# Kernel tuning notes

Measured on AMD Instinct MI355X. Metric: run time of the kernel, lower is better.

The kernel has to match this reference:

```python
import jax, jax.numpy as jnp
import numpy as np

N = 50000          # nodes
E = 1600000        # edges (avg degree 32)
NUM_FEAT = 512
HIDDEN = 128
NUM_CLASS = 40
NUM_LAYERS = 4
EPS = 0.3


def setup_inputs() -> dict:
    key = jax.random.key(0)
    ks = jax.random.split(key, 8)
    x = jax.random.normal(ks[0], (N, NUM_FEAT), dtype=jnp.float32)
    edge_index = jax.random.randint(ks[1], (2, E), 0, N, dtype=jnp.int64)
    gain = 1.414  # xavier_normal_(gain=1.414) as in reset_parameters
    W1 = jax.random.normal(ks[2], (HIDDEN, NUM_FEAT), dtype=jnp.float32) * gain * (2.0 / (HIDDEN + NUM_FEAT)) ** 0.5
    b1 = jnp.zeros((HIDDEN,), dtype=jnp.float32)
    W2 = jax.random.normal(ks[3], (NUM_CLASS, HIDDEN), dtype=jnp.float32) * gain * (2.0 / (NUM_CLASS + HIDDEN)) ** 0.5
    b2 = jnp.zeros((NUM_CLASS,), dtype=jnp.float32)
    # FAConv attention vectors: Linear(channels, 1, bias=False) per layer
    att_l = jax.random.normal(ks[4], (NUM_LAYERS, HIDDEN), dtype=jnp.float32) * (2.0 / (1 + HIDDEN)) ** 0.5
    att_r = jax.random.normal(ks[5], (NUM_LAYERS, HIDDEN), dtype=jnp.float32) * (2.0 / (1 + HIDDEN)) ** 0.5
    return dict(x=x, edge_index=edge_index, W1=W1, b1=b1, W2=W2, b2=b2, att_l=att_l, att_r=att_r)


def reference(x, edge_index, W1, b1, W2, b2, att_l, att_r):
    n = x.shape[0]
    # gcn_norm with self-loops (FAConv default add_self_loops=True)
    loops = jnp.arange(n, dtype=edge_index.dtype)
    src = jnp.concatenate([edge_index[0], loops])  # source j
    dst = jnp.concatenate([edge_index[1], loops])  # target i
    deg = jax.ops.segment_sum(jnp.ones_like(src, dtype=x.dtype), dst, num_segments=n)
    dis = jax.lax.rsqrt(jnp.maximum(deg, 1.0))
    norm = dis[src] * dis[dst]  # [E+N]

    # eval mode: dropout is identity
    h = jax.nn.relu(x @ W1.T + b1)  # [N, HIDDEN]
    raw = h
    for l in range(NUM_LAYERS):
        al = h @ att_l[l]  # [N]
        ar = h @ att_r[l]  # [N]
        coef = jnp.tanh(al[src] + ar[dst]) * norm            # [E+N]
        agg = jax.ops.segment_sum(h[src] * coef[:, None], dst, num_segments=n)
        h = agg + EPS * raw
    logits = h @ W2.T + b2  # [N, NUM_CLASS]
    return jax.nn.log_softmax(logits, axis=1)
```

## Files before the change

kernel.cpp:

```cpp
#include <hip/hip_runtime.h>
#include <cmath>


#define HIDDEN 128
#define FEAT 512
#define NCLASS 40
#define LDST 40
#define NB 256
#define PITCH 12544

typedef __attribute__((ext_vector_type(8))) short short8;
typedef __attribute__((ext_vector_type(4))) float f32x4;

__device__ __forceinline__ float bf_lo(unsigned u) { return __uint_as_float(u << 16); }
__device__ __forceinline__ float bf_hi(unsigned u) { return __uint_as_float(u & 0xffff0000u); }
__device__ __forceinline__ unsigned pack_bf16(float x, float y) {
    unsigned ux = __float_as_uint(x);
    unsigned uy = __float_as_uint(y);
    unsigned lx = (ux + 0x7fffu + ((ux >> 16) & 1u)) >> 16;
    unsigned hy = (uy + 0x7fffu + ((uy >> 16) & 1u)) & 0xffff0000u;
    return hy | lx;
}
__device__ __forceinline__ float fast_tanh(float x) {
    x = fminf(fmaxf(x, -15.f), 15.f);
    float e = __expf(2.f * x);
    return (e - 1.f) / (e + 1.f);
}

__global__ __launch_bounds__(256) void k_hist(const int* __restrict__ ei, int E, int CE,
                                              unsigned* __restrict__ partial,
                                              ushort* __restrict__ lrank) {
    __shared__ unsigned lh[PITCH];
    const int b = blockIdx.x, tid = threadIdx.x;
    for (int w = tid; w < PITCH; w += 256) lh[w] = 0;
    __syncthreads();
    int e0 = b * CE, e1 = min(E, e0 + CE);
    for (int e = e0 + tid; e < e1; e += 256) {
        int dst = ei[E + e];
        int sh = (dst & 3) * 8;
        unsigned old = atomicAdd(&lh[dst >> 2], 1u << sh);
        lrank[e] = (ushort)((old >> sh) & 0xffu);
    }
    __syncthreads();
    unsigned* prow = partial + (size_t)b * PITCH;
    for (int w = tid; w < PITCH; w += 256) prow[w] = lh[w];
}

__global__ void k_hscan(unsigned* __restrict__ partial, int* __restrict__ deg, int n) {
    int w = blockIdx.x * 256 + threadIdx.x;
    if (w >= PITCH) return;
    unsigned run = 0;
    size_t idx = w;
    for (int b = 0; b < NB; ++b, idx += PITCH) {
        unsigned v = partial[idx];
        partial[idx] = run;
        run += v;
    }
    int node = 4 * w;
    if (node < n)     deg[node]     = run & 0xffu;
    if (node + 1 < n) deg[node + 1] = (run >> 8) & 0xffu;
    if (node + 2 < n) deg[node + 2] = (run >> 16) & 0xffu;
    if (node + 3 < n) deg[node + 3] = run >> 24;
}

__global__ void k_dis(const int* __restrict__ deg, float* __restrict__ dis, int n) {
    int i = blockIdx.x * 256 + threadIdx.x;
    if (i < n) dis[i] = rsqrtf((float)(deg[i] + 1));
}

__global__ void k_scan1(const int* __restrict__ deg, int* __restrict__ offs,
                        int* __restrict__ part, int n) {
    __shared__ int s[256];
    int tid = threadIdx.x;
    int gid = blockIdx.x * 256 + tid;
    int v = (gid < n) ? deg[gid] : 0;
    s[tid] = v;
    __syncthreads();
    for (int off = 1; off < 256; off <<= 1) {
        int t = (tid >= off) ? s[tid - off] : 0;
        __syncthreads();
        s[tid] += t;
        __syncthreads();
    }
    if (gid < n) offs[gid] = s[tid] - v;
    if (tid == 255) part[blockIdx.x] = s[255];
}

__global__ void k_scan2(int* __restrict__ part, int nb) {
    __shared__ int s[256];
    int tid = threadIdx.x;
    int v = (tid < nb) ? part[tid] : 0;
    s[tid] = v;
    __syncthreads();
    for (int off = 1; off < 256; off <<= 1) {
        int t = (tid >= off) ? s[tid - off] : 0;
        __syncthreads();
        s[tid] += t;
        __syncthreads();
    }
    if (tid < nb) part[tid] = s[tid] - v;
}

__global__ void k_scan3(int* __restrict__ offs, const int* __restrict__ part, int n, int E) {
    int gid = blockIdx.x * 256 + threadIdx.x;
    if (gid < n) offs[gid] += part[blockIdx.x];
    if (gid == 0) offs[n] = E;
}

__global__ __launch_bounds__(256) void k_csr_fill(const int* __restrict__ ei, int E, int CE,
                                                  const int* __restrict__ offs,
                                                  const unsigned* __restrict__ partial,
                                                  const ushort* __restrict__ lrank,
                                                  int* __restrict__ csrc) {
    __shared__ unsigned lp[PITCH];
    const int b = blockIdx.x, tid = threadIdx.x;
    const unsigned* prow = partial + (size_t)b * PITCH;
    for (int w = tid; w < PITCH; w += 256) lp[w] = prow[w];
    __syncthreads();
    int e0 = b * CE, e1 = min(E, e0 + CE);
    for (int e = e0 + tid; e < e1; e += 256) {
        int dst = ei[E + e];
        int src = ei[e];
        unsigned wv = lp[dst >> 2];
        int base = (wv >> ((dst & 3) * 8)) & 0xffu;
        csrc[offs[dst] + base + (int)lrank[e]] = src;
    }
}

__global__ __launch_bounds__(256) void k_gemm1(const float* __restrict__ x,
                                               const float* __restrict__ W1,
                                               const float* __restrict__ b1,
                                               float* __restrict__ h, int M) {
    __shared__ ushort As[128 * LDST];
    __shared__ ushort Bs[128 * LDST];
    const int tid = threadIdx.x;
    const int bm = blockIdx.x * 128;
    const int wave = tid >> 6, lane = tid & 63;
    const int rh = (wave >> 1) * 64;
    const int ch = (wave & 1) * 64;
    const int sub = lane & 15, quad = lane >> 4;
    const int lrow = tid >> 3;
    const int lcol = (tid & 7) * 4;
    f32x4 acc[4][4] = {};
    for (int k0 = 0; k0 < FEAT; k0 += 32) {
#pragma unroll
        for (int i = 0; i < 4; ++i) {
            int r = lrow + 32 * i;
            int grow = bm + r;
            float4 v = make_float4(0.f, 0.f, 0.f, 0.f);
            if (grow < M) v = *(const float4*)(x + (size_t)grow * FEAT + k0 + lcol);
            uint2 pk = make_uint2(pack_bf16(v.x, v.y), pack_bf16(v.z, v.w));
            *(uint2*)(As + r * LDST + lcol) = pk;
        }
#pragma unroll
        for (int i = 0; i < 4; ++i) {
            int r = lrow + 32 * i;
            float4 v = *(const float4*)(W1 + (size_t)r * FEAT + k0 + lcol);
            uint2 pk = make_uint2(pack_bf16(v.x, v.y), pack_bf16(v.z, v.w));
            *(uint2*)(Bs + r * LDST + lcol) = pk;
        }
        __syncthreads();
        short8 af[4], bfr[4];
#pragma unroll
        for (int t = 0; t < 4; ++t)
            af[t] = *(const short8*)(As + (rh + t * 16 + sub) * LDST + quad * 8);
#pragma unroll
        for (int u = 0; u < 4; ++u)
            bfr[u] = *(const short8*)(Bs + (ch + u * 16 + sub) * LDST + quad * 8);
#pragma unroll
        for (int t = 0; t < 4; ++t)
#pragma unroll
            for (int u = 0; u < 4; ++u)
                acc[t][u] = __builtin_amdgcn_mfma_f32_16x16x32_bf16(af[t], bfr[u], acc[t][u], 0, 0, 0);
        __syncthreads();
    }
    float b1v[4];
#pragma unroll
    for (int u = 0; u < 4; ++u) b1v[u] = b1[ch + u * 16 + sub];
#pragma unroll
    for (int t = 0; t < 4; ++t) {
#pragma unroll
        for (int u = 0; u < 4; ++u) {
            int col = ch + u * 16 + sub;
#pragma unroll
            for (int r2 = 0; r2 < 4; ++r2) {
                int grow = bm + rh + t * 16 + quad * 4 + r2;
                if (grow < M)
                    h[(size_t)grow * HIDDEN + col] = fmaxf(acc[t][u][r2] + b1v[u], 0.f);
            }
        }
    }
}

__global__ void k_prep(const float* __restrict__ h, unsigned* __restrict__ hbf,
                       const float* __restrict__ attl, const float* __restrict__ attr,
                       const float* __restrict__ dis, float2* __restrict__ al2,
                       float* __restrict__ ar, int n) {
    int node = (blockIdx.x * blockDim.x + threadIdx.x) >> 6;
    int lane = threadIdx.x & 63;
    if (node >= n) return;
    float2 hv = ((const float2*)(h + (size_t)node * HIDDEN))[lane];
    hbf[(size_t)node * 64 + lane] = pack_bf16(hv.x, hv.y);
    float pl = hv.x * attl[2 * lane] + hv.y * attl[2 * lane + 1];
    float pr = hv.x * attr[2 * lane] + hv.y * attr[2 * lane + 1];
    for (int off = 32; off; off >>= 1) {
        pl += __shfl_down(pl, off);
        pr += __shfl_down(pr, off);
    }
    if (lane == 0) {
        al2[node] = make_float2(pl, dis[node]);
        ar[node] = pr;
    }
}

__global__ void k_aggregate(const unsigned* __restrict__ hbf, const float* __restrict__ raw,
                            const float2* __restrict__ al2, const float* __restrict__ ar,
                            const int* __restrict__ offs, const int* __restrict__ csrc,
                            float* __restrict__ hout, unsigned* __restrict__ houtbf,
                            const float* __restrict__ attl_n, const float* __restrict__ attr_n,
                            float2* __restrict__ al2_o, float* __restrict__ ar_o, int n) {
    int node = (blockIdx.x * blockDim.x + threadIdx.x) >> 6;
    int lane = threadIdx.x & 63;
    if (node >= n) return;
    const int grp = lane >> 4;
    const int sub = lane & 15;
    const float arn = ar[node];
    const float2 selfld = al2[node];
    const float disn = selfld.y;
    float acc[8] = {0.f, 0.f, 0.f, 0.f, 0.f, 0.f, 0.f, 0.f};
    int e0 = offs[node], e1 = offs[node + 1];
    int e = e0;
    for (; e + 16 <= e1; e += 16) {
        int smy = csrc[e + sub];
        float2 lmy = al2[smy];
        float cmy = fast_tanh(lmy.x + arn) * lmy.y * disn;
        int sa = __shfl(smy, grp);
        int sb = __shfl(smy, 4 + grp);
        int sc = __shfl(smy, 8 + grp);
        int sd = __shfl(smy, 12 + grp);
        float ca = __shfl(cmy, grp);
        float cb = __shfl(cmy, 4 + grp);
        float cc = __shfl(cmy, 8 + grp);
        float cd = __shfl(cmy, 12 + grp);
        uint4 ra = *(const uint4*)(hbf + (size_t)sa * 64 + sub * 4);
        uint4 rb = *(const uint4*)(hbf + (size_t)sb * 64 + sub * 4);
        uint4 rc = *(const uint4*)(hbf + (size_t)sc * 64 + sub * 4);
        uint4 rd = *(const uint4*)(hbf + (size_t)sd * 64 + sub * 4);
        acc[0] += ca * bf_lo(ra.x); acc[1] += ca * bf_hi(ra.x);
        acc[2] += ca * bf_lo(ra.y); acc[3] += ca * bf_hi(ra.y);
        acc[4] += ca * bf_lo(ra.z); acc[5] += ca * bf_hi(ra.z);
        acc[6] += ca * bf_lo(ra.w); acc[7] += ca * bf_hi(ra.w);
        acc[0] += cb * bf_lo(rb.x); acc[1] += cb * bf_hi(rb.x);
        acc[2] += cb * bf_lo(rb.y); acc[3] += cb * bf_hi(rb.y);
        acc[4] += cb * bf_lo(rb.z); acc[5] += cb * bf_hi(rb.z);
        acc[6] += cb * bf_lo(rb.w); acc[7] += cb * bf_hi(rb.w);
        acc[0] += cc * bf_lo(rc.x); acc[1] += cc * bf_hi(rc.x);
        acc[2] += cc * bf_lo(rc.y); acc[3] += cc * bf_hi(rc.y);
        acc[4] += cc * bf_lo(rc.z); acc[5] += cc * bf_hi(rc.z);
        acc[6] += cc * bf_lo(rc.w); acc[7] += cc * bf_hi(rc.w);
        acc[0] += cd * bf_lo(rd.x); acc[1] += cd * bf_hi(rd.x);
        acc[2] += cd * bf_lo(rd.y); acc[3] += cd * bf_hi(rd.y);
        acc[4] += cd * bf_lo(rd.z); acc[5] += cd * bf_hi(rd.z);
        acc[6] += cd * bf_lo(rd.w); acc[7] += cd * bf_hi(rd.w);
    }
    for (; e + 4 <= e1; e += 4) {
        int sa = csrc[e + grp];
        float2 la = al2[sa];
        uint4 ra = *(const uint4*)(hbf + (size_t)sa * 64 + sub * 4);
        float ca = fast_tanh(la.x + arn) * la.y * disn;
        acc[0] += ca * bf_lo(ra.x); acc[1] += ca * bf_hi(ra.x);
        acc[2] += ca * bf_lo(ra.y); acc[3] += ca * bf_hi(ra.y);
        acc[4] += ca * bf_lo(ra.z); acc[5] += ca * bf_hi(ra.z);
        acc[6] += ca * bf_lo(ra.w); acc[7] += ca * bf_hi(ra.w);
    }
#pragma unroll
    for (int j = 0; j < 8; ++j) {
        acc[j] += __shfl_xor(acc[j], 16);
        acc[j] += __shfl_xor(acc[j], 32);
    }
    for (; e < e1; ++e) {
        int s = csrc[e];
        float2 ls = al2[s];
        uint4 r = *(const uint4*)(hbf + (size_t)s * 64 + sub * 4);
        float c = fast_tanh(ls.x + arn) * ls.y * disn;
        acc[0] += c * bf_lo(r.x); acc[1] += c * bf_hi(r.x);
        acc[2] += c * bf_lo(r.y); acc[3] += c * bf_hi(r.y);
        acc[4] += c * bf_lo(r.z); acc[5] += c * bf_hi(r.z);
        acc[6] += c * bf_lo(r.w); acc[7] += c * bf_hi(r.w);
    }
    {
        float c = fast_tanh(selfld.x + arn) * disn * disn;
        uint4 r = *(const uint4*)(hbf + (size_t)node * 64 + sub * 4);
        acc[0] += c * bf_lo(r.x); acc[1] += c * bf_hi(r.x);
        acc[2] += c * bf_lo(r.y); acc[3] += c * bf_hi(r.y);
        acc[4] += c * bf_lo(r.z); acc[5] += c * bf_hi(r.z);
        acc[6] += c * bf_lo(r.w); acc[7] += c * bf_hi(r.w);
    }
    float o[8];
    {
        float4 rv0 = *(const float4*)(raw + (size_t)node * HIDDEN + sub * 8);
        float4 rv1 = *(const float4*)(raw + (size_t)node * HIDDEN + sub * 8 + 4);
        o[0] = acc[0] + 0.3f * rv0.x; o[1] = acc[1] + 0.3f * rv0.y;
        o[2] = acc[2] + 0.3f * rv0.z; o[3] = acc[3] + 0.3f * rv0.w;
        o[4] = acc[4] + 0.3f * rv1.x; o[5] = acc[5] + 0.3f * rv1.y;
        o[6] = acc[6] + 0.3f * rv1.z; o[7] = acc[7] + 0.3f * rv1.w;
    }
    if (grp == 0) {
        *(float4*)(hout + (size_t)node * HIDDEN + sub * 8) = make_float4(o[0], o[1], o[2], o[3]);
        *(float4*)(hout + (size_t)node * HIDDEN + sub * 8 + 4) = make_float4(o[4], o[5], o[6], o[7]);
        if (houtbf) {
            uint4 pk = make_uint4(pack_bf16(o[0], o[1]), pack_bf16(o[2], o[3]),
                                  pack_bf16(o[4], o[5]), pack_bf16(o[6], o[7]));
            *(uint4*)(houtbf + (size_t)node * 64 + sub * 4) = pk;
        }
    }
    if (attl_n) {
        float4 a0 = *(const float4*)(attl_n + sub * 8);
        float4 a1 = *(const float4*)(attl_n + sub * 8 + 4);
        float4 c0 = *(const float4*)(attr_n + sub * 8);
        float4 c1 = *(const float4*)(attr_n + sub * 8 + 4);
        float pl = o[0] * a0.x + o[1] * a0.y + o[2] * a0.z + o[3] * a0.w +
                   o[4] * a1.x + o[5] * a1.y + o[6] * a1.z + o[7] * a1.w;
        float pr = o[0] * c0.x + o[1] * c0.y + o[2] * c0.z + o[3] * c0.w +
                   o[4] * c1.x + o[5] * c1.y + o[6] * c1.z + o[7] * c1.w;
        for (int off = 8; off; off >>= 1) {
            pl += __shfl_xor(pl, off);
            pr += __shfl_xor(pr, off);
        }
        if (lane == 0) {
            al2_o[node] = make_float2(pl, disn);
            ar_o[node] = pr;
        }
    }
}

__global__ __launch_bounds__(256) void k_out(const float* __restrict__ h,
                                             const float* __restrict__ W2,
                                             const float* __restrict__ b2,
                                             float* __restrict__ out, int n) {
    __shared__ float ws[NCLASS * HIDDEN];
    __shared__ float bs[NCLASS];
    const int tid = threadIdx.x;
    for (int i = tid; i < NCLASS * HIDDEN / 4; i += 256)
        ((float4*)ws)[i] = ((const float4*)W2)[i];
    if (tid < NCLASS) bs[tid] = b2[tid];
    __syncthreads();
    int node = blockIdx.x * 128 + (tid >> 1);
    const int half = tid & 1;
    const int c0 = half * 20;
    if (node >= n) return;
    const float* hr = h + (size_t)node * HIDDEN;
    float acc[20];
#pragma unroll
    for (int c = 0; c < 20; ++c) acc[c] = bs[c0 + c];
#pragma unroll
    for (int k0 = 0; k0 < HIDDEN; k0 += 16) {
        float4 h0 = *(const float4*)(hr + k0);
        float4 h1 = *(const float4*)(hr + k0 + 4);
        float4 h2v = *(const float4*)(hr + k0 + 8);
        float4 h3 = *(const float4*)(hr + k0 + 12);
#pragma unroll
        for (int c = 0; c < 20; ++c) {
            const float* w = ws + (c0 + c) * HIDDEN + k0;
            float4 w0 = *(const float4*)(w);
            float4 w1 = *(const float4*)(w + 4);
            float4 w2v = *(const float4*)(w + 8);
            float4 w3 = *(const float4*)(w + 12);
            acc[c] += h0.x * w0.x + h0.y * w0.y + h0.z * w0.z + h0.w * w0.w +
                      h1.x * w1.x + h1.y * w1.y + h1.z * w1.z + h1.w * w1.w +
                      h2v.x * w2v.x + h2v.y * w2v.y + h2v.z * w2v.z + h2v.w * w2v.w +
                      h3.x * w3.x + h3.y * w3.y + h3.z * w3.z + h3.w * w3.w;
        }
    }
    float m = -INFINITY;
#pragma unroll
    for (int c = 0; c < 20; ++c) m = fmaxf(m, acc[c]);
    m = fmaxf(m, __shfl_xor(m, 1));
    float ssum = 0.f;
#pragma unroll
    for (int c = 0; c < 20; ++c) ssum += expf(acc[c] - m);
    ssum += __shfl_xor(ssum, 1);
    float lse = m + logf(ssum);
    float* orow = out + (size_t)node * NCLASS + c0;
#pragma unroll
    for (int c = 0; c < 20; ++c) orow[c] = acc[c] - lse;
}

extern "C" void kernel_launch(void* const* d_in, const int* in_sizes, int n_in,
                              void* d_out, int out_size, void* d_ws, size_t ws_size,
                              hipStream_t stream) {
    const float* x    = (const float*)d_in[0];
    const int*   ei   = (const int*)d_in[1];
    const float* W1   = (const float*)d_in[2];
    const float* b1   = (const float*)d_in[3];
    const float* W2   = (const float*)d_in[4];
    const float* b2   = (const float*)d_in[5];
    const float* attl = (const float*)d_in[6];
    const float* attr = (const float*)d_in[7];
    const int N = in_sizes[0] / FEAT;
    const int E = in_sizes[1] / 2;
    float* out = (float*)d_out;

    char* p = (char*)d_ws;
    auto take = [&](size_t bytes) {
        void* q = (void*)p;
        p += (bytes + 255) & ~(size_t)255;
        return q;
    };
    float*    h0   = (float*)take((size_t)N * HIDDEN * 4);
    float*    h1   = (float*)take((size_t)N * HIDDEN * 4);
    float*    h2   = (float*)take((size_t)N * HIDDEN * 4);
    unsigned* hb0  = (unsigned*)take((size_t)N * 64 * 4);
    unsigned* hb1  = (unsigned*)take((size_t)N * 64 * 4);
    int*      deg  = (int*)take((size_t)N * 4);
    float*    dis  = (float*)take((size_t)N * 4);
    int*      offs = (int*)take((size_t)(N + 1) * 4);
    unsigned* partial = (unsigned*)take((size_t)NB * PITCH * 4);
    ushort*   lrank   = (ushort*)take((size_t)E * 2);
    int*      csrc = (int*)take((size_t)E * 4);
    float2*   al2A = (float2*)take((size_t)N * 8);
    float2*   al2B = (float2*)take((size_t)N * 8);
    float*    arA  = (float*)take((size_t)N * 4);
    float*    arB  = (float*)take((size_t)N * 4);
    int*      part = (int*)take(1024);

    const int nbl = (N + 255) / 256;
    const int CE = (E + NB - 1) / NB;

    k_hist<<<NB, 256, 0, stream>>>(ei, E, CE, partial, lrank);
    k_hscan<<<(PITCH + 255) / 256, 256, 0, stream>>>(partial, deg, N);
    k_dis<<<nbl, 256, 0, stream>>>(deg, dis, N);
    k_scan1<<<nbl, 256, 0, stream>>>(deg, offs, part, N);
    k_scan2<<<1, 256, 0, stream>>>(part, nbl);
    k_scan3<<<nbl, 256, 0, stream>>>(offs, part, N, E);
    k_csr_fill<<<NB, 256, 0, stream>>>(ei, E, CE, offs, partial, lrank, csrc);

    k_gemm1<<<(N + 127) / 128, 256, 0, stream>>>(x, W1, b1, h0, N);
    k_prep<<<(N + 3) / 4, 256, 0, stream>>>(h0, hb0, attl, attr, dis, al2A, arA, N);

    float*    fout[4] = {h1, h2, h1, h2};
    unsigned* hbin = hb0, *hbout = hb1;
    float2*   alin = al2A, *alout = al2B;
    float*    arin = arA,  *arout = arB;
    for (int l = 0; l < 4; ++l) {
        const float* attl_n = (l < 3) ? (attl + (l + 1) * HIDDEN) : nullptr;
        const float* attr_n = (l < 3) ? (attr + (l + 1) * HIDDEN) : nullptr;
        unsigned* hbo = (l < 3) ? hbout : nullptr;
        k_aggregate<<<(N + 3) / 4, 256, 0, stream>>>(hbin, h0, alin, arin, offs, csrc,
                                                     fout[l], hbo, attl_n, attr_n,
                                                     alout, arout, N);
        unsigned* tb = hbin; hbin = hbout; hbout = tb;
        float2* ta = alin; alin = alout; alout = ta;
        float* tr = arin; arin = arout; arout = tr;
    }

    k_out<<<(N + 127) / 128, 256, 0, stream>>>(h2, W2, b2, out, N);
}
```

Before: 579.1 us.

## Halve GEMM1 row tile and prefetch next K-slice into registers

The first-layer GEMM kernel now uses 64-row tiles instead of 128, doubling the block count (about 782 blocks for 50000 nodes) to fill more compute units. It also software-pipelines the K loop by loading the next 32-wide slice of x and W1 into registers while the current slice's MFMAs run. The aim is to hide global-memory latency in a GEMM bound by bandwidth on reading x. In exchange, W1 is re-read by twice as many blocks and each block does less MFMA work per load.

```diff
diff --git a/kernel.cpp b/kernel.cpp
--- a/kernel.cpp
+++ b/kernel.cpp
@@ -8,6 +8,7 @@
 #define LDST 40
 #define NB 256
 #define PITCH 12544
+#define BM1 64
 
 typedef __attribute__((ext_vector_type(8))) short short8;
 typedef __attribute__((ext_vector_type(4))) float f32x4;
@@ -131,44 +132,59 @@
                                                const float* __restrict__ W1,
                                                const float* __restrict__ b1,
                                                float* __restrict__ h, int M) {
-    __shared__ ushort As[128 * LDST];
+    __shared__ ushort As[BM1 * LDST];
     __shared__ ushort Bs[128 * LDST];
     const int tid = threadIdx.x;
-    const int bm = blockIdx.x * 128;
+    const int bm = blockIdx.x * BM1;
     const int wave = tid >> 6, lane = tid & 63;
-    const int rh = (wave >> 1) * 64;
+    const int rh = (wave >> 1) * 32;
     const int ch = (wave & 1) * 64;
     const int sub = lane & 15, quad = lane >> 4;
     const int lrow = tid >> 3;
     const int lcol = (tid & 7) * 4;
-    f32x4 acc[4][4] = {};
+    f32x4 acc[2][4] = {};
+    float4 av[2], bv[4];
+#pragma unroll
+    for (int i = 0; i < 2; ++i) {
+        int grow = bm + lrow + 32 * i;
+        av[i] = (grow < M) ? *(const float4*)(x + (size_t)grow * FEAT + lcol)
+                           : make_float4(0.f, 0.f, 0.f, 0.f);
+    }
+#pragma unroll
+    for (int i = 0; i < 4; ++i)
+        bv[i] = *(const float4*)(W1 + (size_t)(lrow + 32 * i) * FEAT + lcol);
+
     for (int k0 = 0; k0 < FEAT; k0 += 32) {
 #pragma unroll
-        for (int i = 0; i < 4; ++i) {
-            int r = lrow + 32 * i;
-            int grow = bm + r;
-            float4 v = make_float4(0.f, 0.f, 0.f, 0.f);
-            if (grow < M) v = *(const float4*)(x + (size_t)grow * FEAT + k0 + lcol);
-            uint2 pk = make_uint2(pack_bf16(v.x, v.y), pack_bf16(v.z, v.w));
-            *(uint2*)(As + r * LDST + lcol) = pk;
-        }
-#pragma unroll
-        for (int i = 0; i < 4; ++i) {
-            int r = lrow + 32 * i;
-            float4 v = *(const float4*)(W1 + (size_t)r * FEAT + k0 + lcol);
-            uint2 pk = make_uint2(pack_bf16(v.x, v.y), pack_bf16(v.z, v.w));
-            *(uint2*)(Bs + r * LDST + lcol) = pk;
-        }
-        __syncthreads();
-        short8 af[4], bfr[4];
-#pragma unroll
-        for (int t = 0; t < 4; ++t)
+        for (int i = 0; i < 2; ++i)
+            *(uint2*)(As + (lrow + 32 * i) * LDST + lcol) =
+                make_uint2(pack_bf16(av[i].x, av[i].y), pack_bf16(av[i].z, av[i].w));
+#pragma unroll
+        for (int i = 0; i < 4; ++i)
+            *(uint2*)(Bs + (lrow + 32 * i) * LDST + lcol) =
+                make_uint2(pack_bf16(bv[i].x, bv[i].y), pack_bf16(bv[i].z, bv[i].w));
+        __syncthreads();
+        if (k0 + 32 < FEAT) {
+            const int kn = k0 + 32;
+#pragma unroll
+            for (int i = 0; i < 2; ++i) {
+                int grow = bm + lrow + 32 * i;
+                av[i] = (grow < M) ? *(const float4*)(x + (size_t)grow * FEAT + kn + lcol)
+                                   : make_float4(0.f, 0.f, 0.f, 0.f);
+            }
+#pragma unroll
+            for (int i = 0; i < 4; ++i)
+                bv[i] = *(const float4*)(W1 + (size_t)(lrow + 32 * i) * FEAT + kn + lcol);
+        }
+        short8 af[2], bfr[4];
+#pragma unroll
+        for (int t = 0; t < 2; ++t)
             af[t] = *(const short8*)(As + (rh + t * 16 + sub) * LDST + quad * 8);
 #pragma unroll
         for (int u = 0; u < 4; ++u)
             bfr[u] = *(const short8*)(Bs + (ch + u * 16 + sub) * LDST + quad * 8);
 #pragma unroll
-        for (int t = 0; t < 4; ++t)
+        for (int t = 0; t < 2; ++t)
 #pragma unroll
             for (int u = 0; u < 4; ++u)
                 acc[t][u] = __builtin_amdgcn_mfma_f32_16x16x32_bf16(af[t], bfr[u], acc[t][u], 0, 0, 0);
@@ -178,7 +194,7 @@
 #pragma unroll
     for (int u = 0; u < 4; ++u) b1v[u] = b1[ch + u * 16 + sub];
 #pragma unroll
-    for (int t = 0; t < 4; ++t) {
+    for (int t = 0; t < 2; ++t) {
 #pragma unroll
         for (int u = 0; u < 4; ++u) {
             int col = ch + u * 16 + sub;
@@ -435,7 +451,7 @@
     k_scan3<<<nbl, 256, 0, stream>>>(offs, part, N, E);
     k_csr_fill<<<NB, 256, 0, stream>>>(ei, E, CE, offs, partial, lrank, csrc);
 
-    k_gemm1<<<(N + 127) / 128, 256, 0, stream>>>(x, W1, b1, h0, N);
+    k_gemm1<<<(N + BM1 - 1) / BM1, 256, 0, stream>>>(x, W1, b1, h0, N);
     k_prep<<<(N + 3) / 4, 256, 0, stream>>>(h0, hb0, attl, attr, dis, al2A, arA, N);
 
     float*    fout[4] = {h1, h2, h1, h2};
```

New measurement: 565.0 us. 2.4% less time.
